# Optimization experiments

Hardware: AMD Instinct MI355X
Metric: run time of the kernel (lower is better)

The kernel has to match this reference:

```python
import jax, jax.numpy as jnp
import numpy as np

B, LD = 256, 64
NO, LO = 10240, 32
NM, LM = 81920, 16
EO, EM = 81920, 327680
E, HID, H, Dh, V = 128, 256, 8, 16, 10000


def masked_mean(tokens, table):
    # tokens: [N, L] int; pad id = 0
    emb = table[tokens]                            # [N, L, E]
    mask = (tokens != 0)
    s = jnp.sum(emb * mask[..., None].astype(emb.dtype), axis=1)
    lens = jnp.maximum(jnp.sum(mask, axis=1), 1).astype(emb.dtype)
    return s / lens[:, None]


def segment_softmax(scores, seg, num_segments):
    # scores: [E, ...]; softmax over entries sharing seg id (PyG softmax)
    m = jax.ops.segment_max(scores, seg, num_segments=num_segments)
    e = jnp.exp(scores - m[seg])
    s = jax.ops.segment_sum(e, seg, num_segments=num_segments)
    return e / (s[seg] + 1e-16)


def gcn_conv(x, W, b, src, dst, n):
    # PyG GCNConv: normalize=True, add_self_loops=True
    xw = x @ W
    loops = jnp.arange(n, dtype=src.dtype)
    s2 = jnp.concatenate([src, loops])
    d2 = jnp.concatenate([dst, loops])
    deg = jax.ops.segment_sum(jnp.ones_like(d2, dtype=x.dtype), d2, num_segments=n)
    dinv = deg ** -0.5  # deg >= 1 due to self loops
    norm = dinv[s2] * dinv[d2]
    out = jax.ops.segment_sum(xw[s2] * norm[:, None], d2, num_segments=n)
    return out + b


def transformer_conv(x, Wq, bq, Wk, bk, Wv, bv, Wskip, bskip, src, dst, n):
    q = (x @ Wq + bq).reshape(n, H, Dh)
    k = (x @ Wk + bk).reshape(n, H, Dh)
    v = (x @ Wv + bv).reshape(n, H, Dh)
    score = jnp.sum(q[dst] * k[src], axis=-1) / jnp.sqrt(jnp.asarray(Dh, x.dtype))  # [E, H]
    alpha = segment_softmax(score, dst, n)
    agg = jax.ops.segment_sum(alpha[:, :, None] * v[src], dst, num_segments=n)  # [n, H, Dh]
    return agg.reshape(n, H * Dh) + x @ Wskip + bskip


def global_attention(x, Wg, bg, seg, num_segments):
    gate = x @ Wg + bg                              # [N, 1]
    a = segment_softmax(gate, seg, num_segments)
    return jax.ops.segment_sum(a * x, seg, num_segments=num_segments)


def setup_inputs():
    key = jax.random.key(0)
    ks = jax.random.split(key, 20)
    sc = lambda k, shape: jax.random.normal(k, shape, dtype=jnp.float32) * 0.05
    inp = {
        "desc_tokens": jax.random.randint(ks[0], (B, LD), 0, V, dtype=jnp.int32),
        "x_tokens": jax.random.randint(ks[1], (NO, LO), 0, V, dtype=jnp.int32),
        "mini_tokens": jax.random.randint(ks[2], (NM, LM), 0, V, dtype=jnp.int32),
        "src": jax.random.randint(ks[3], (EO,), 0, NO, dtype=jnp.int32),
        "dst": jax.random.randint(ks[4], (EO,), 0, NO, dtype=jnp.int32),
        "mini_src": jax.random.randint(ks[5], (EM,), 0, NM, dtype=jnp.int32),
        "mini_dst": jax.random.randint(ks[6], (EM,), 0, NM, dtype=jnp.int32),
        "mini_batch": (jnp.arange(NM, dtype=jnp.int32) // (NM // NO)),
        "node_batch": (jnp.arange(NO, dtype=jnp.int32) // (NO // B)),
        "desc_table": sc(ks[7], (V, E)),
        "code_table": sc(ks[8], (V, E)),
        "code_table2": sc(ks[9], (V, E)),
        "Wq": sc(ks[10], (E, H * Dh)), "bq": jnp.zeros((H * Dh,), jnp.float32),
        "Wk": sc(ks[11], (E, H * Dh)), "bk": jnp.zeros((H * Dh,), jnp.float32),
        "Wv": sc(ks[12], (E, H * Dh)), "bv": jnp.zeros((H * Dh,), jnp.float32),
        "Wskip": sc(ks[13], (E, H * Dh)), "bskip": jnp.zeros((H * Dh,), jnp.float32),
        "W2": sc(ks[14], (E, HID)), "b2": jnp.zeros((HID,), jnp.float32),
        "W3": sc(ks[15], (HID, E)), "b3": jnp.zeros((E,), jnp.float32),
        "Wg": sc(ks[16], (E, 1)), "bg": jnp.zeros((1,), jnp.float32),
    }
    return inp


def reference(desc_tokens, x_tokens, mini_tokens, src, dst, mini_src, mini_dst,
              mini_batch, node_batch, desc_table, code_table, code_table2,
              Wq, bq, Wk, bk, Wv, bv, Wskip, bskip, W2, b2, W3, b3, Wg, bg):
    # encode_desc: embedding + masked mean pool -> [B, E]
    h_n = masked_mean(desc_tokens, desc_table)
    # encode_code_graph
    stmt_emb = masked_mean(x_tokens, code_table2)          # [NO, E]
    mini_emb = masked_mean(mini_tokens, code_table)        # [NM, E]
    mini_hidden = transformer_conv(mini_emb, Wq, bq, Wk, bk, Wv, bv,
                                   Wskip, bskip, mini_src, mini_dst, NM)
    mini_fn = global_attention(mini_hidden, Wg, bg, mini_batch, NO)  # [NO, E]
    mini_fn = (mini_fn + stmt_emb) * 0.5
    h = jax.nn.relu(gcn_conv(mini_fn, W2, b2, src, dst, NO))
    final_stmt = gcn_conv(h, W3, b3, src, dst, NO)
    fn_repr = global_attention(final_stmt, Wg, bg, node_batch, B)    # [B, E]
    # cosine similarity (torch eps=1e-8 clamps each norm)
    na = jnp.maximum(jnp.linalg.norm(fn_repr, axis=-1), 1e-8)
    nb = jnp.maximum(jnp.linalg.norm(h_n, axis=-1), 1e-8)
    return jnp.sum(fn_repr * h_n, axis=-1) / (na * nb)
```

## Files before the change

kernel.cpp:

```cpp
#include <hip/hip_runtime.h>
#include <hip/hip_bf16.h>
#include <math.h>

#define BB   256
#define LDE  64
#define NO   10240
#define LO   32
#define NM   81920
#define LM   16
#define EO   81920
#define EM   327680
#define ED   128
#define HIDD 256
#define NH   8
#define DH   16
#define VV   10000

static inline int nblk(long long n, int b) { return (int)((n + b - 1) / b); }

typedef __attribute__((ext_vector_type(8))) short short8;
typedef __attribute__((ext_vector_type(4))) float f32x4;

static __device__ __forceinline__ unsigned short bf16_rne(float f) {
  unsigned u = __float_as_uint(f);
  return (unsigned short)((u + 0x7fffu + ((u >> 16) & 1u)) >> 16);
}
static __device__ __forceinline__ float bf16_to_f(unsigned short h) {
  return __uint_as_float(((unsigned)h) << 16);
}
static __device__ __forceinline__ float4 b4f(ushort4 h) {
  return make_float4(bf16_to_f(h.x), bf16_to_f(h.y), bf16_to_f(h.z), bf16_to_f(h.w));
}
static __device__ __forceinline__ ushort4 f4b(float4 v) {
  return make_ushort4(bf16_rne(v.x), bf16_rne(v.y), bf16_rne(v.z), bf16_rne(v.w));
}

struct ConvArgs {
  const float *Wq, *Wk, *Wv, *Ws, *W2, *W3;
  const float *bq, *bk, *bv, *bs;
  short8* frag;
  float* bias512;
  const float* t1; unsigned short* o1;
  const float* t2; unsigned short* o2;
  int* hist;
};
#define TBLK (2 * VV * ED / 4 / 256)
#define ZBLK ((NM + NO) / 256)
__global__ void __launch_bounds__(256)
conv_all_k(ConvArgs A) {
  int b = blockIdx.x;
  if (b < 32) {
    int g = b * 256 + threadIdx.x;
    int lane = g & 63, fid = g >> 6;
    int nt = fid & 31, kb = fid >> 5;
    int c = nt * 16 + (lane & 15);
    int k0 = kb * 32 + ((lane >> 4) << 3);
    const float* wp; int cm;
    if (c < 128)      { wp = A.Wq; cm = c; }
    else if (c < 384) { int u = c - 128, t = u & 7;
                        wp = (t < 4) ? A.Wk : A.Wv; cm = (u >> 3) * 4 + (t & 3); }
    else              { wp = A.Ws; cm = c - 384; }
    short8 h;
    #pragma unroll
    for (int j = 0; j < 8; ++j)
      h[j] = (short)bf16_rne(wp[(size_t)(k0 + j) * 128 + cm]);
    A.frag[g] = h;
  } else if (b < 64) {
    int g = (b - 32) * 256 + threadIdx.x;
    const float* wp; int M, dstbase, gg;
    if (g < 4096) { wp = A.W2; M = 256; dstbase = 8192;  gg = g; }
    else          { wp = A.W3; M = 128; dstbase = 12288; gg = g - 4096; }
    int lane = gg & 63, fid = gg >> 6;
    int nt = fid % (M / 16), kb = fid / (M / 16);
    int n = nt * 16 + (lane & 15);
    int k0 = kb * 32 + ((lane >> 4) << 3);
    short8 h;
    #pragma unroll
    for (int j = 0; j < 8; ++j)
      h[j] = (short)bf16_rne(wp[(size_t)(k0 + j) * M + n]);
    A.frag[dstbase + gg] = h;
  } else if (b < 64 + TBLK) {
    int q = (b - 64) * 256 + threadIdx.x;
    const int NT = VV * ED / 4;
    if (q < NT) {
      float4 v = *(const float4*)(A.t1 + (size_t)q * 4);
      *(ushort4*)(A.o1 + (size_t)q * 4) = f4b(v);
    } else if (q < 2 * NT) {
      int q2 = q - NT;
      float4 v = *(const float4*)(A.t2 + (size_t)q2 * 4);
      *(ushort4*)(A.o2 + (size_t)q2 * 4) = f4b(v);
    }
  } else if (b < 64 + TBLK + ZBLK) {
    int i = (b - 64 - TBLK) * 256 + threadIdx.x;
    if (i < NM + NO) A.hist[i] = 0;
  } else {
    for (int c = threadIdx.x; c < 512; c += 256) {
      float v;
      if (c < 128)      v = A.bq[c];
      else if (c < 384) { int u = c - 128, t = u & 7;
                          v = (t < 4) ? A.bk[(u >> 3) * 4 + t] : A.bv[(u >> 3) * 4 + (t & 3)]; }
      else              v = A.bs[c - 384];
      A.bias512[c] = v;
    }
  }
}

template<int L>
static __device__ __forceinline__ void embed_body_f(const int* __restrict__ tokens,
                                                    const float* __restrict__ table,
                                                    float* __restrict__ out, int blk) {
  const int r = threadIdx.x >> 5, lane = threadIdx.x & 31;
  const int n0 = blk * 8;
  __shared__ int toks[8][L];
  for (int i = threadIdx.x; i < 8 * L; i += 256)
    toks[i / L][i % L] = tokens[(size_t)n0 * L + i];
  __syncthreads();
  float4 acc = make_float4(0.f, 0.f, 0.f, 0.f);
  int cnt = 0;
  #pragma unroll
  for (int l = 0; l < L; ++l) {
    int t = toks[r][l];
    float4 v = *(const float4*)(table + (size_t)t * ED + lane * 4);
    float msk = (t != 0) ? 1.f : 0.f;
    cnt += (t != 0);
    acc.x = fmaf(msk, v.x, acc.x); acc.y = fmaf(msk, v.y, acc.y);
    acc.z = fmaf(msk, v.z, acc.z); acc.w = fmaf(msk, v.w, acc.w);
  }
  float inv = 1.f / (float)(cnt > 0 ? cnt : 1);
  acc.x *= inv; acc.y *= inv; acc.z *= inv; acc.w *= inv;
  *(float4*)(out + (size_t)(n0 + r) * ED + lane * 4) = acc;
}

template<int L>
static __device__ __forceinline__ void embed_body16(const int* __restrict__ tokens,
                                                    const unsigned short* __restrict__ table,
                                                    unsigned short* __restrict__ out, int blk) {
  const int r = threadIdx.x >> 4, lane = threadIdx.x & 15;
  const int n0 = blk * 16;
  __shared__ int toks[16][L];
  for (int i = threadIdx.x; i < 16 * L; i += 256)
    toks[i / L][i % L] = tokens[(size_t)n0 * L + i];
  __syncthreads();
  float acc[8] = {};
  int cnt = 0;
  #pragma unroll
  for (int l = 0; l < L; ++l) {
    int t = toks[r][l];
    short8 v = *(const short8*)(table + (size_t)t * ED + lane * 8);
    float msk = (t != 0) ? 1.f : 0.f;
    cnt += (t != 0);
    #pragma unroll
    for (int j = 0; j < 8; ++j)
      acc[j] = fmaf(msk, bf16_to_f((unsigned short)v[j]), acc[j]);
  }
  float inv = 1.f / (float)(cnt > 0 ? cnt : 1);
  short8 o;
  #pragma unroll
  for (int j = 0; j < 8; ++j) o[j] = (short)bf16_rne(acc[j] * inv);
  *(short8*)(out + (size_t)(n0 + r) * ED + lane * 8) = o;
}

__global__ void __launch_bounds__(256)
embed_all_k(const int* __restrict__ desc_tokens, const float* __restrict__ desc_table,
            float* __restrict__ h_n,
            const int* __restrict__ x_tokens, const unsigned short* __restrict__ ctab2,
            unsigned short* __restrict__ stmt,
            const int* __restrict__ mini_tokens, const unsigned short* __restrict__ ctab,
            unsigned short* __restrict__ miniE) {
  int b = blockIdx.x;
  if (b < BB / 8) embed_body_f<LDE>(desc_tokens, desc_table, h_n, b);
  else if (b < BB / 8 + NO / 16) embed_body16<LO>(x_tokens, ctab2, stmt, b - BB / 8);
  else embed_body16<LM>(mini_tokens, ctab, miniE, b - BB / 8 - NO / 16);
}

__global__ void __launch_bounds__(512)
qkvs_merged_k(const unsigned short* __restrict__ Ab, const short8* __restrict__ Wf,
              const float* __restrict__ bias512, unsigned short* __restrict__ out) {
  const int id = blockIdx.x;
  const int blk = (id & 7) * 80 + (id >> 3);
  const int n0 = blk * 128;
  const int tid = threadIdx.x;
  const int w = tid >> 6, lane = tid & 63;
  const int r = lane & 15, qd = lane >> 4;
  const int node = n0 + w * 16 + r;
  __shared__ unsigned short lds[8 * 16 * 128];
  char* myl = (char*)(lds + w * 2048);

  short8 a[4];
  #pragma unroll
  for (int kb = 0; kb < 4; ++kb)
    a[kb] = *(const short8*)(Ab + (size_t)node * ED + kb * 32 + qd * 8);

  #pragma unroll
  for (int ch = 0; ch < 4; ++ch) {
    #pragma unroll 4
    for (int jl = 0; jl < 8; ++jl) {
      const int cf = ch * 8 + jl;
      f32x4 acc = (f32x4){0.f, 0.f, 0.f, 0.f};
      #pragma unroll
      for (int kb = 0; kb < 4; ++kb) {
        short8 wf = Wf[((size_t)(kb * 32 + cf)) * 64 + lane];
        acc = __builtin_amdgcn_mfma_f32_16x16x32_bf16(wf, a[kb], acc, 0, 0, 0);
      }
      const int colb = cf * 16 + qd * 4;
      const float4 bv = *(const float4*)(bias512 + colb);
      ushort4 o;
      o.x = bf16_rne(acc[0] + bv.x);
      o.y = bf16_rne(acc[1] + bv.y);
      o.z = bf16_rne(acc[2] + bv.z);
      o.w = bf16_rne(acc[3] + bv.w);
      *(ushort4*)(myl + r * 256 + (((jl * 32) ^ ((r & 7) << 5)) + qd * 8)) = o;
    }
    #pragma unroll
    for (int t = 0; t < 4; ++t) {
      const int rr = t * 4 + qd;
      const int o16 = (lane & 15) * 16;
      short8 v = *(const short8*)(myl + rr * 256 + (o16 ^ ((rr & 7) << 5)));
      *(short8*)(out + (size_t)(n0 + w * 16 + rr) * 512 + ch * 128 + (lane & 15) * 8) = v;
    }
  }
}

template<bool RELU>
__global__ void __launch_bounds__(512)
mgemm_b_k(const unsigned short* __restrict__ Ab, const short8* __restrict__ Bh,
          const float* __restrict__ bias, unsigned short* __restrict__ C,
          int K, int M) {
  const int bn0 = blockIdx.x * 128;
  const int n0 = blockIdx.y * 128;
  const int tid = threadIdx.x;
  const int w = tid >> 6, lane = tid & 63;
  const int wm = (w & 3) * 2, wn = (w >> 2) * 4;
  const int r = lane & 15, qd = lane >> 4;
  const int NTm = M / 16;
  f32x4 acc[2][4];
  #pragma unroll
  for (int i = 0; i < 2; ++i)
    #pragma unroll
    for (int j = 0; j < 4; ++j) acc[i][j] = (f32x4){0.f, 0.f, 0.f, 0.f};
  const int kbn = K / 32;
  for (int kb = 0; kb < kbn; ++kb) {
    short8 bh[4];
    #pragma unroll
    for (int j = 0; j < 4; ++j)
      bh[j] = Bh[((size_t)kb * NTm + (bn0 >> 4) + wn + j) * 64 + lane];
    short8 a[2];
    #pragma unroll
    for (int i = 0; i < 2; ++i)
      a[i] = *(const short8*)(Ab + (size_t)(n0 + (wm + i) * 16 + r) * K + kb * 32 + qd * 8);
    #pragma unroll
    for (int i = 0; i < 2; ++i)
      #pragma unroll
      for (int j = 0; j < 4; ++j)
        acc[i][j] = __builtin_amdgcn_mfma_f32_16x16x32_bf16(bh[j], a[i], acc[i][j], 0, 0, 0);
  }
  #pragma unroll
  for (int i = 0; i < 2; ++i)
    #pragma unroll
    for (int j = 0; j < 4; ++j) {
      const int node = n0 + (wm + i) * 16 + r;
      const int colb = bn0 + (wn + j) * 16 + qd * 4;
      float4 bv = bias ? *(const float4*)(bias + colb) : make_float4(0.f, 0.f, 0.f, 0.f);
      float v0 = acc[i][j][0] + bv.x;
      float v1 = acc[i][j][1] + bv.y;
      float v2 = acc[i][j][2] + bv.z;
      float v3 = acc[i][j][3] + bv.w;
      if (RELU) {
        v0 = fmaxf(v0, 0.f); v1 = fmaxf(v1, 0.f);
        v2 = fmaxf(v2, 0.f); v3 = fmaxf(v3, 0.f);
      }
      ushort4 o = make_ushort4(bf16_rne(v0), bf16_rne(v1), bf16_rne(v2), bf16_rne(v3));
      *(ushort4*)(C + (size_t)node * M + colb) = o;
    }
}

__global__ void hist2_k(const int* __restrict__ dm, int* __restrict__ hm,
                        const int* __restrict__ dd, int* __restrict__ ho) {
  int e = blockIdx.x * 256 + threadIdx.x;
  if (e < EM) atomicAdd(&hm[dm[e]], 1);
  else { int e2 = e - EM; if (e2 < EO) atomicAdd(&ho[dd[e2]], 1); }
}
__global__ void chunk_sum_k(const int* __restrict__ hist, int* __restrict__ partials, int N) {
  __shared__ int sd[256];
  int i = blockIdx.x * 256 + threadIdx.x;
  sd[threadIdx.x] = (i < N) ? hist[i] : 0;
  __syncthreads();
  for (int s = 128; s > 0; s >>= 1) {
    if (threadIdx.x < s) sd[threadIdx.x] += sd[threadIdx.x + s];
    __syncthreads();
  }
  if (threadIdx.x == 0) partials[blockIdx.x] = sd[0];
}
__global__ void scan_partials2_k(int* __restrict__ p) {
  __shared__ int sd[512];
  int base = (blockIdx.x == 0) ? 0 : NM / 256;
  int B    = (blockIdx.x == 0) ? NM / 256 : NO / 256;
  int t = threadIdx.x;
  int v = (t < B) ? p[base + t] : 0;
  sd[t] = v; __syncthreads();
  for (int off = 1; off < 512; off <<= 1) {
    int a = (t >= off) ? sd[t - off] : 0;
    __syncthreads();
    sd[t] += a;
    __syncthreads();
  }
  if (t < B) p[base + t] = sd[t] - v;
}
__global__ void scan_final2_k(const int* __restrict__ hist, const int* __restrict__ partials,
                              int* __restrict__ offsm, int* __restrict__ curm,
                              int* __restrict__ offso, int* __restrict__ curo,
                              float* __restrict__ dinv) {
  __shared__ int sd[256];
  int i = blockIdx.x * 256 + threadIdx.x;
  int v = hist[i];
  sd[threadIdx.x] = v; __syncthreads();
  for (int off = 1; off < 256; off <<= 1) {
    int a = (threadIdx.x >= off) ? sd[threadIdx.x - off] : 0;
    __syncthreads();
    sd[threadIdx.x] += a;
    __syncthreads();
  }
  int excl = sd[threadIdx.x] - v + partials[blockIdx.x];
  if (i < NM) {
    offsm[i] = excl; curm[i] = excl;
    if (i == NM - 1) offsm[NM] = excl + v;
  } else {
    int i2 = i - NM;
    offso[i2] = excl; curo[i2] = excl;
    if (i2 == NO - 1) offso[NO] = excl + v;
    dinv[i2] = 1.f / sqrtf(1.f + (float)v);
  }
}
__global__ void scatter2_k(const int* __restrict__ sm, const int* __restrict__ dm,
                           int* __restrict__ cm, int* __restrict__ km,
                           const int* __restrict__ so, const int* __restrict__ dd,
                           int* __restrict__ co, int* __restrict__ ko) {
  int e = blockIdx.x * 256 + threadIdx.x;
  if (e < EM) {
    int pos = atomicAdd(&cm[dm[e]], 1);
    km[pos] = sm[e];
  } else {
    int e2 = e - EM;
    if (e2 < EO) {
      int pos = atomicAdd(&co[dd[e2]], 1);
      ko[pos] = so[e2];
    }
  }
}

__global__ void __launch_bounds__(128)
attn_fused_k(unsigned short* buf,
             const int* __restrict__ offs, const int* __restrict__ csr,
             const float* __restrict__ Wg, const float* __restrict__ bg,
             float* __restrict__ gateOut) {
  const int g = threadIdx.x >> 5, lane = threadIdx.x & 31;
  const int n = blockIdx.x * 4 + g;
  float4 q = b4f(*(const ushort4*)(buf + (size_t)n * 512 + lane * 4));
  int lo = offs[n], hi = offs[n + 1];
  float4 O = make_float4(0.f, 0.f, 0.f, 0.f);
  float m = -INFINITY, l = 0.f;
  for (int base = lo; base < hi; base += 4) {
    int rem = hi - base;
    int sidx[4];
    #pragma unroll
    for (int i = 0; i < 4; ++i) sidx[i] = (i < rem) ? csr[base + i] : 0;
    short8 kvr[4];
    #pragma unroll
    for (int i = 0; i < 4; ++i)
      kvr[i] = *(const short8*)(buf + (size_t)sidx[i] * 512 + 128 + lane * 8);
    #pragma unroll
    for (int i = 0; i < 4; ++i) {
      float4 kt = make_float4(bf16_to_f((unsigned short)kvr[i][0]),
                              bf16_to_f((unsigned short)kvr[i][1]),
                              bf16_to_f((unsigned short)kvr[i][2]),
                              bf16_to_f((unsigned short)kvr[i][3]));
      float4 vt = make_float4(bf16_to_f((unsigned short)kvr[i][4]),
                              bf16_to_f((unsigned short)kvr[i][5]),
                              bf16_to_f((unsigned short)kvr[i][6]),
                              bf16_to_f((unsigned short)kvr[i][7]));
      float p = q.x * kt.x + q.y * kt.y + q.z * kt.z + q.w * kt.w;
      p += __shfl_xor(p, 1, 64);
      p += __shfl_xor(p, 2, 64);
      float sc = (i < rem) ? p * 0.25f : -INFINITY;
      float mn = fmaxf(m, sc);
      float scale = __expf(m - mn);
      float pe = __expf(sc - mn);
      l = l * scale + pe;
      O.x = O.x * scale + pe * vt.x; O.y = O.y * scale + pe * vt.y;
      O.z = O.z * scale + pe * vt.z; O.w = O.w * scale + pe * vt.w;
      m = mn;
    }
  }
  float inv = 1.f / (l + 1e-16f);
  float4 sk = b4f(*(const ushort4*)(buf + (size_t)n * 512 + 384 + lane * 4));
  float4 out = make_float4(O.x * inv + sk.x, O.y * inv + sk.y,
                           O.z * inv + sk.z, O.w * inv + sk.w);
  *(ushort4*)(buf + (size_t)n * 512 + lane * 4) = f4b(out);
  float4 wg = *(const float4*)(Wg + lane * 4);
  float ps = out.x * wg.x + out.y * wg.y + out.z * wg.z + out.w * wg.w;
  #pragma unroll
  for (int o = 1; o <= 16; o <<= 1) ps += __shfl_xor(ps, o, 64);
  if (lane == 0) gateOut[n] = ps + bg[0];
}

__global__ void __launch_bounds__(256)
gcn_gather_b_k(const unsigned short* __restrict__ x, const float* __restrict__ dinv,
               const int* __restrict__ offs, const int* __restrict__ csr,
               const float* __restrict__ bias, unsigned short* __restrict__ out,
               const float* __restrict__ Wg, const float* __restrict__ bg,
               float* __restrict__ gateOut) {
  const int wv = threadIdx.x >> 6, lane = threadIdx.x & 63;
  const int half = lane >> 5, cl = lane & 31;
  const int n = blockIdx.x * 4 + wv;
  float di = dinv[n];
  float4 acc = make_float4(0.f, 0.f, 0.f, 0.f);
  if (half == 0) {
    float4 xs = b4f(*(const ushort4*)(x + (size_t)n * ED + cl * 4));
    float w0 = di * di;
    acc = make_float4(w0 * xs.x, w0 * xs.y, w0 * xs.z, w0 * xs.w);
  }
  int lo = offs[n], hi = offs[n + 1];
  for (int base = lo; base < hi; base += 8) {
    int sidx[4]; bool ok[4];
    #pragma unroll
    for (int i = 0; i < 4; ++i) {
      int e = base + 2 * i + half;
      ok[i] = e < hi;
      sidx[i] = ok[i] ? csr[e] : 0;
    }
    float dw[4];
    #pragma unroll
    for (int i = 0; i < 4; ++i) dw[i] = ok[i] ? di * dinv[sidx[i]] : 0.f;
    ushort4 vr[4];
    #pragma unroll
    for (int i = 0; i < 4; ++i)
      vr[i] = *(const ushort4*)(x + (size_t)sidx[i] * ED + cl * 4);
    #pragma unroll
    for (int i = 0; i < 4; ++i) {
      float4 v = b4f(vr[i]);
      acc.x = fmaf(dw[i], v.x, acc.x); acc.y = fmaf(dw[i], v.y, acc.y);
      acc.z = fmaf(dw[i], v.z, acc.z); acc.w = fmaf(dw[i], v.w, acc.w);
    }
  }
  acc.x += __shfl_xor(acc.x, 32, 64); acc.y += __shfl_xor(acc.y, 32, 64);
  acc.z += __shfl_xor(acc.z, 32, 64); acc.w += __shfl_xor(acc.w, 32, 64);
  if (bias) {
    float4 b4 = *(const float4*)(bias + cl * 4);
    acc.x += b4.x; acc.y += b4.y; acc.z += b4.z; acc.w += b4.w;
  }
  if (half == 0)
    *(ushort4*)(out + (size_t)n * ED + cl * 4) = f4b(acc);
  if (gateOut) {
    float4 wg = *(const float4*)(Wg + cl * 4);
    float ps = acc.x * wg.x + acc.y * wg.y + acc.z * wg.z + acc.w * wg.w;
    #pragma unroll
    for (int o = 1; o <= 16; o <<= 1) ps += __shfl_xor(ps, o, 64);
    if (lane == 0) gateOut[n] = ps + bg[0];
  }
}

static __device__ __forceinline__ int lower_bound_d(const int* a, int n, int key) {
  int lo = 0, hi = n;
  while (lo < hi) { int mid = (lo + hi) >> 1; if (a[mid] < key) lo = mid + 1; else hi = mid; }
  return lo;
}
__global__ void __launch_bounds__(128)
gattn_comb_b_k(const unsigned short* __restrict__ xv, const float* __restrict__ gate,
               const int* __restrict__ seg, int Ntot,
               const unsigned short* __restrict__ other, unsigned short* __restrict__ out) {
  const int g = threadIdx.x >> 5, lane = threadIdx.x & 31;
  const int n = blockIdx.x * 4 + g;
  __shared__ int sh[4][2];
  if (lane == 0) {
    sh[g][0] = lower_bound_d(seg, Ntot, n);
    sh[g][1] = lower_bound_d(seg, Ntot, n + 1);
  }
  __syncthreads();
  int lo = sh[g][0], hi = sh[g][1];
  float m = -INFINITY;
  for (int j = lo; j < hi; ++j) m = fmaxf(m, gate[j]);
  float ssum = 0.f;
  for (int j = lo; j < hi; ++j) ssum += __expf(gate[j] - m);
  float inv = 1.f / (ssum + 1e-16f);
  float4 acc = make_float4(0.f, 0.f, 0.f, 0.f);
  for (int j = lo; j < hi; ++j) {
    float a = __expf(gate[j] - m) * inv;
    float4 v = b4f(*(const ushort4*)(xv + (size_t)j * 512 + lane * 4));
    acc.x = fmaf(a, v.x, acc.x); acc.y = fmaf(a, v.y, acc.y);
    acc.z = fmaf(a, v.z, acc.z); acc.w = fmaf(a, v.w, acc.w);
  }
  float4 o4 = b4f(*(const ushort4*)(other + (size_t)n * ED + lane * 4));
  acc.x = (acc.x + o4.x) * 0.5f; acc.y = (acc.y + o4.y) * 0.5f;
  acc.z = (acc.z + o4.z) * 0.5f; acc.w = (acc.w + o4.w) * 0.5f;
  *(ushort4*)(out + (size_t)n * ED + lane * 4) = f4b(acc);
}

__global__ void __launch_bounds__(128)
gattn_cos_k(const unsigned short* __restrict__ x, const float* __restrict__ gate,
            const int* __restrict__ seg, int Ntot,
            const float* __restrict__ hn, float* __restrict__ outp) {
  const int g = threadIdx.x >> 5, lane = threadIdx.x & 31;
  const int n = blockIdx.x * 4 + g;
  __shared__ int sh[4][2];
  if (lane == 0) {
    sh[g][0] = lower_bound_d(seg, Ntot, n);
    sh[g][1] = lower_bound_d(seg, Ntot, n + 1);
  }
  __syncthreads();
  int lo = sh[g][0], hi = sh[g][1];
  float m = -INFINITY;
  for (int j = lo; j < hi; ++j) m = fmaxf(m, gate[j]);
  float ssum = 0.f;
  for (int j = lo; j < hi; ++j) ssum += __expf(gate[j] - m);
  float inv = 1.f / (ssum + 1e-16f);
  float4 acc = make_float4(0.f, 0.f, 0.f, 0.f);
  for (int j = lo; j < hi; ++j) {
    float a = __expf(gate[j] - m) * inv;
    float4 v = b4f(*(const ushort4*)(x + (size_t)j * ED + lane * 4));
    acc.x = fmaf(a, v.x, acc.x); acc.y = fmaf(a, v.y, acc.y);
    acc.z = fmaf(a, v.z, acc.z); acc.w = fmaf(a, v.w, acc.w);
  }
  float4 hv = *(const float4*)(hn + (size_t)n * ED + lane * 4);
  float dot = acc.x * hv.x + acc.y * hv.y + acc.z * hv.z + acc.w * hv.w;
  float na  = acc.x * acc.x + acc.y * acc.y + acc.z * acc.z + acc.w * acc.w;
  float nb  = hv.x * hv.x + hv.y * hv.y + hv.z * hv.z + hv.w * hv.w;
  #pragma unroll
  for (int o = 1; o <= 16; o <<= 1) {
    dot += __shfl_xor(dot, o, 64);
    na  += __shfl_xor(na,  o, 64);
    nb  += __shfl_xor(nb,  o, 64);
  }
  if (lane == 0)
    outp[n] = dot / (fmaxf(sqrtf(na), 1e-8f) * fmaxf(sqrtf(nb), 1e-8f));
}

constexpr size_t OFF_HN    = 0;
constexpr size_t OFF_STMT  = OFF_HN    + (size_t)BB * ED;
constexpr size_t OFF_A     = OFF_STMT  + (size_t)NO * ED;
constexpr size_t OFF_CT    = OFF_A     + (size_t)NM * ED;
constexpr size_t OFF_QKVS  = OFF_CT    + (size_t)VV * ED;
constexpr size_t T0        = OFF_QKVS  + (size_t)NM * 256;
constexpr size_t OFF_GATE  = T0;
constexpr size_t OFF_GATE2 = OFF_GATE  + (size_t)NM;
constexpr size_t OFF_DINV  = OFF_GATE2 + (size_t)NO;
constexpr size_t OFF_HISTM = OFF_DINV  + (size_t)NO;
constexpr size_t OFF_HISTO = OFF_HISTM + (size_t)NM;
constexpr size_t OFF_OFFSM = OFF_HISTO + (size_t)NO;
constexpr size_t OFF_CURM  = OFF_OFFSM + (size_t)NM + 1;
constexpr size_t OFF_CSRM  = OFF_CURM  + (size_t)NM;
constexpr size_t OFF_OFFSO = OFF_CSRM  + (size_t)EM;
constexpr size_t OFF_CURO  = OFF_OFFSO + (size_t)NO + 1;
constexpr size_t OFF_CSRO  = OFF_CURO  + (size_t)NO;
constexpr size_t OFF_PART  = OFF_CSRO  + (size_t)EO;
constexpr size_t OFF_B512  = OFF_PART  + 512;
constexpr size_t OFF_WFHI  = OFF_B512  + 512;
constexpr size_t OFF_MFN   = OFF_A;
constexpr size_t OFF_AGG   = OFF_MFN   + (size_t)NO * ED;
constexpr size_t OFF_H     = OFF_AGG   + (size_t)NO * ED;
constexpr size_t OFF_T     = OFF_H     + (size_t)NO * HIDD;
constexpr size_t OFF_FIN   = OFF_T     + (size_t)NO * ED;

extern "C" void kernel_launch(void* const* d_in, const int* in_sizes, int n_in,
                              void* d_out, int out_size, void* d_ws, size_t ws_size,
                              hipStream_t stream) {
  const int* desc_tokens = (const int*)d_in[0];
  const int* x_tokens    = (const int*)d_in[1];
  const int* mini_tokens = (const int*)d_in[2];
  const int* src         = (const int*)d_in[3];
  const int* dst         = (const int*)d_in[4];
  const int* mini_src    = (const int*)d_in[5];
  const int* mini_dst    = (const int*)d_in[6];
  const int* mini_batch  = (const int*)d_in[7];
  const int* node_batch  = (const int*)d_in[8];
  const float* desc_table  = (const float*)d_in[9];
  const float* code_table  = (const float*)d_in[10];
  const float* code_table2 = (const float*)d_in[11];
  const float* Wq = (const float*)d_in[12]; const float* bq = (const float*)d_in[13];
  const float* Wk = (const float*)d_in[14]; const float* bk = (const float*)d_in[15];
  const float* Wv = (const float*)d_in[16]; const float* bv = (const float*)d_in[17];
  const float* Wskip = (const float*)d_in[18]; const float* bskip = (const float*)d_in[19];
  const float* W2 = (const float*)d_in[20]; const float* b2 = (const float*)d_in[21];
  const float* W3 = (const float*)d_in[22]; const float* b3 = (const float*)d_in[23];
  const float* Wg = (const float*)d_in[24]; const float* bg = (const float*)d_in[25];

  float* ws = (float*)d_ws;
  float* h_n   = ws + OFF_HN;
  unsigned short* stmt_b  = (unsigned short*)(ws + OFF_STMT);
  unsigned short* miniE_b = (unsigned short*)(ws + OFF_A);
  unsigned short* ctab_b  = (unsigned short*)(ws + OFF_CT);
  unsigned short* ctab2_b = ctab_b + (size_t)VV * ED;
  unsigned short* qkvs_b  = (unsigned short*)(ws + OFF_QKVS);
  float* gate  = ws + OFF_GATE;
  float* gate2 = ws + OFF_GATE2;
  float* dinv  = ws + OFF_DINV;
  int* histm = (int*)(ws + OFF_HISTM);
  int* histo = (int*)(ws + OFF_HISTO);
  int* offsm = (int*)(ws + OFF_OFFSM);
  int* curm  = (int*)(ws + OFF_CURM);
  int* csrm  = (int*)(ws + OFF_CSRM);
  int* offso = (int*)(ws + OFF_OFFSO);
  int* curo  = (int*)(ws + OFF_CURO);
  int* csro  = (int*)(ws + OFF_CSRO);
  int* part  = (int*)(ws + OFF_PART);
  float* bias512 = ws + OFF_B512;
  short8* wfrag = (short8*)(ws + OFF_WFHI);
  unsigned short* mini_fn_b = (unsigned short*)(ws + OFF_MFN);
  unsigned short* aggb_b    = (unsigned short*)(ws + OFF_AGG);
  unsigned short* hbuf_b    = (unsigned short*)(ws + OFF_H);
  unsigned short* tbuf_b    = (unsigned short*)(ws + OFF_T);
  unsigned short* finalS_b  = (unsigned short*)(ws + OFF_FIN);
  float* outp    = (float*)d_out;

  ConvArgs ca;
  ca.Wq = Wq; ca.Wk = Wk; ca.Wv = Wv; ca.Ws = Wskip; ca.W2 = W2; ca.W3 = W3;
  ca.bq = bq; ca.bk = bk; ca.bv = bv; ca.bs = bskip;
  ca.frag = wfrag; ca.bias512 = bias512;
  ca.t1 = code_table;  ca.o1 = ctab_b;
  ca.t2 = code_table2; ca.o2 = ctab2_b;
  ca.hist = histm;
  conv_all_k<<<64 + TBLK + ZBLK + 1, 256, 0, stream>>>(ca);

  hist2_k<<<nblk(EM + EO, 256), 256, 0, stream>>>(mini_dst, histm, dst, histo);
  chunk_sum_k<<<(NM + NO) / 256, 256, 0, stream>>>(histm, part, NM + NO);
  scan_partials2_k<<<2, 512, 0, stream>>>(part);
  scan_final2_k<<<(NM + NO) / 256, 256, 0, stream>>>(histm, part, offsm, curm,
                                                     offso, curo, dinv);
  scatter2_k<<<nblk(EM + EO, 256), 256, 0, stream>>>(mini_src, mini_dst, curm, csrm,
                                                     src, dst, curo, csro);

  embed_all_k<<<BB / 8 + NO / 16 + NM / 16, 256, 0, stream>>>(
      desc_tokens, desc_table, h_n, x_tokens, ctab2_b, stmt_b,
      mini_tokens, ctab_b, miniE_b);

  qkvs_merged_k<<<NM / 128, 512, 0, stream>>>(miniE_b, wfrag, bias512, qkvs_b);

  attn_fused_k<<<NM / 4, 128, 0, stream>>>(qkvs_b, offsm, csrm, Wg, bg, gate);

  gattn_comb_b_k<<<NO / 4, 128, 0, stream>>>(qkvs_b, gate, mini_batch, NM,
                                             stmt_b, mini_fn_b);

  gcn_gather_b_k<<<NO / 4, 256, 0, stream>>>(mini_fn_b, dinv, offso, csro, nullptr,
                                             aggb_b, nullptr, nullptr, nullptr);
  { dim3 g(HIDD / 128, NO / 128);
    mgemm_b_k<true><<<g, 512, 0, stream>>>(aggb_b, wfrag + 8192, b2, hbuf_b, ED, HIDD); }

  { dim3 g(1, NO / 128);
    mgemm_b_k<false><<<g, 512, 0, stream>>>(hbuf_b, wfrag + 12288, nullptr, tbuf_b, HIDD, ED); }
  gcn_gather_b_k<<<NO / 4, 256, 0, stream>>>(tbuf_b, dinv, offso, csro, b3, finalS_b,
                                             Wg, bg, gate2);

  gattn_cos_k<<<BB / 4, 128, 0, stream>>>(finalS_b, gate2, node_batch, NO, h_n, outp);
}
```

Before: 342.5 us.

## Stage QKVS weight fragments in LDS via global_load_lds and repack layout

Weight fragments for the merged QKV/skip GEMM are reordered so that each output chunk's fragments are contiguous. Each chunk is then bulk-copied into shared memory with global_load_lds, and all waves read it from LDS instead of each wave fetching weights from global memory per MFMA. The output staging buffer is shrunk to half-chunk tiles with padded rows in place of XOR swizzling. This adds two block barriers per chunk and drops full loop unrolling.

```diff
diff --git a/kernel.cpp b/kernel.cpp
--- a/kernel.cpp
+++ b/kernel.cpp
@@ -33,6 +33,12 @@
 }
 static __device__ __forceinline__ ushort4 f4b(float4 v) {
   return make_ushort4(bf16_rne(v.x), bf16_rne(v.y), bf16_rne(v.z), bf16_rne(v.w));
+}
+
+static __device__ __forceinline__ void gl_lds16(const void* g, void* l) {
+  __builtin_amdgcn_global_load_lds(
+      (const __attribute__((address_space(1))) unsigned int*)g,
+      (__attribute__((address_space(3))) unsigned int*)l, 16, 0, 0);
 }
 
 struct ConvArgs {
@@ -51,9 +57,10 @@
   int b = blockIdx.x;
   if (b < 32) {
     int g = b * 256 + threadIdx.x;
-    int lane = g & 63, fid = g >> 6;
-    int nt = fid & 31, kb = fid >> 5;
-    int c = nt * 16 + (lane & 15);
+    int lane = g & 63, f = g >> 6;
+    int jl = f & 7, kb = (f >> 3) & 3, ch = f >> 5;
+    int cf = ch * 8 + jl;
+    int c = cf * 16 + (lane & 15);
     int k0 = kb * 32 + ((lane >> 4) << 3);
     const float* wp; int cm;
     if (c < 128)      { wp = A.Wq; cm = c; }
@@ -183,41 +190,56 @@
   const int w = tid >> 6, lane = tid & 63;
   const int r = lane & 15, qd = lane >> 4;
   const int node = n0 + w * 16 + r;
-  __shared__ unsigned short lds[8 * 16 * 128];
-  char* myl = (char*)(lds + w * 2048);
+  __shared__ short8 wlds[2048];
+  __shared__ short8 elds[8 * 144];
+  char* myl = (char*)elds + w * 2304;
 
   short8 a[4];
   #pragma unroll
   for (int kb = 0; kb < 4; ++kb)
     a[kb] = *(const short8*)(Ab + (size_t)node * ED + kb * 32 + qd * 8);
 
-  #pragma unroll
   for (int ch = 0; ch < 4; ++ch) {
-    #pragma unroll 4
-    for (int jl = 0; jl < 8; ++jl) {
-      const int cf = ch * 8 + jl;
-      f32x4 acc = (f32x4){0.f, 0.f, 0.f, 0.f};
+    {
+      const char* gs = (const char*)Wf + (size_t)ch * 32768
+                     + (size_t)(w * 4) * 1024 + (size_t)lane * 16;
+      char* ls = (char*)wlds + (w * 4) * 1024;
       #pragma unroll
-      for (int kb = 0; kb < 4; ++kb) {
-        short8 wf = Wf[((size_t)(kb * 32 + cf)) * 64 + lane];
-        acc = __builtin_amdgcn_mfma_f32_16x16x32_bf16(wf, a[kb], acc, 0, 0, 0);
+      for (int t = 0; t < 4; ++t)
+        gl_lds16(gs + t * 1024, ls + t * 1024);
+    }
+    __syncthreads();
+
+    #pragma unroll
+    for (int hf = 0; hf < 2; ++hf) {
+      #pragma unroll
+      for (int j4 = 0; j4 < 4; ++j4) {
+        const int jl = hf * 4 + j4;
+        f32x4 acc = (f32x4){0.f, 0.f, 0.f, 0.f};
+        #pragma unroll
+        for (int kb = 0; kb < 4; ++kb) {
+          short8 wf = *(const short8*)((const char*)wlds
+                        + ((size_t)((kb << 3) | jl) * 64 + lane) * 16);
+          acc = __builtin_amdgcn_mfma_f32_16x16x32_bf16(wf, a[kb], acc, 0, 0, 0);
+        }
+        const int cf = ch * 8 + jl;
+        const float4 bv = *(const float4*)(bias512 + cf * 16 + qd * 4);
+        ushort4 o;
+        o.x = bf16_rne(acc[0] + bv.x);
+        o.y = bf16_rne(acc[1] + bv.y);
+        o.z = bf16_rne(acc[2] + bv.z);
+        o.w = bf16_rne(acc[3] + bv.w);
+        *(ushort4*)(myl + r * 144 + j4 * 32 + qd * 8) = o;
       }
-      const int colb = cf * 16 + qd * 4;
-      const float4 bv = *(const float4*)(bias512 + colb);
-      ushort4 o;
-      o.x = bf16_rne(acc[0] + bv.x);
-      o.y = bf16_rne(acc[1] + bv.y);
-      o.z = bf16_rne(acc[2] + bv.z);
-      o.w = bf16_rne(acc[3] + bv.w);
-      *(ushort4*)(myl + r * 256 + (((jl * 32) ^ ((r & 7) << 5)) + qd * 8)) = o;
-    }
-    #pragma unroll
-    for (int t = 0; t < 4; ++t) {
-      const int rr = t * 4 + qd;
-      const int o16 = (lane & 15) * 16;
-      short8 v = *(const short8*)(myl + rr * 256 + (o16 ^ ((rr & 7) << 5)));
-      *(short8*)(out + (size_t)(n0 + w * 16 + rr) * 512 + ch * 128 + (lane & 15) * 8) = v;
-    }
+      #pragma unroll
+      for (int t = 0; t < 2; ++t) {
+        const int rr = t * 8 + (lane >> 3);
+        short8 v = *(const short8*)(myl + rr * 144 + (lane & 7) * 16);
+        *(short8*)(out + (size_t)(n0 + w * 16 + rr) * 512
+                   + ch * 128 + hf * 64 + (lane & 7) * 8) = v;
+      }
+    }
+    __syncthreads();
   }
 }
 
```

After: 328.7 us. 4.0% less time.
